# Performance work log

Measured on AMD Instinct MI355X. Metric: run time of the kernel, lower is better.

## Reference

```python
import jax, jax.numpy as jnp
import numpy as np
import math

C_CURV = 1.0          # manifold curvature c
KH = KW = 3
STRIDE = (1, 1)
PADDING = (1, 1)
DILATION = (1, 1)
IN_CH = 64            # includes time channel
OUT_CH = 64           # excludes time channel


def setup_inputs() -> dict:
    key = jax.random.key(0)
    k1, k2, k3 = jax.random.split(key, 3)
    B, H, W = 32, 64, 64
    x = jax.random.normal(k1, (B, H, W, IN_CH), dtype=jnp.float32)
    kk = KH * KW
    lin_in = (IN_CH - 1) * kk + 1  # 568
    stdv = math.sqrt(2.0 / ((IN_CH - 1) * kk))
    weight = jax.random.uniform(k2, (OUT_CH, lin_in), minval=-stdv, maxval=stdv, dtype=jnp.float32)
    bias = jax.random.uniform(k3, (OUT_CH,), minval=-stdv, maxval=stdv, dtype=jnp.float32)
    return {"x": x, "weight": weight, "bias": bias}


def _im2col(x):
    """x: [B,H,W,C] -> gathered patches [B,h_out,w_out,KH,KW,C] (torch Unfold semantics)."""
    B, H, W, C = x.shape
    xp = jnp.pad(x, ((0, 0), (PADDING[0], PADDING[0]), (PADDING[1], PADDING[1]), (0, 0)))
    h_out = (H + 2 * PADDING[0] - DILATION[0] * (KH - 1) - 1) // STRIDE[0] + 1
    w_out = (W + 2 * PADDING[1] - DILATION[1] * (KW - 1) - 1) // STRIDE[1] + 1
    rows = STRIDE[0] * jnp.arange(h_out)[:, None] + DILATION[0] * jnp.arange(KH)[None, :]  # [h_out,KH]
    cols = STRIDE[1] * jnp.arange(w_out)[:, None] + DILATION[1] * jnp.arange(KW)[None, :]  # [w_out,KW]
    g = xp[:, rows[:, None, :, None], cols[None, :, None, :], :]  # [B,h_out,w_out,KH,KW,C]
    return g, h_out, w_out


def reference(x, weight, bias):
    B = x.shape[0]
    kk = KH * KW
    g, h_out, w_out = _im2col(x)
    L = h_out * w_out
    # Time channel (channel 0) over kernel positions, clamped to sqrt(c)
    t = jnp.maximum(g[..., 0].reshape(B, L, kk), jnp.sqrt(jnp.float32(C_CURV)))
    t_rescaled = jnp.sqrt(jnp.sum(t * t, axis=-1, keepdims=True) - (kk - 1) * C_CURV)
    # Space channels in kernel-major, channel-minor order (matches torch reshape/transpose)
    s = g[..., 1:].reshape(B, L, kk * (IN_CH - 1))
    feat = jnp.concatenate([t_rescaled, s], axis=-1)  # [B, L, 568]
    # LorentzLinear: linear on features, recompute time from space norm
    y_space = jnp.einsum('blf,of->blo', feat, weight) + bias
    y_time = jnp.sqrt(jnp.sum(y_space * y_space, axis=-1, keepdims=True) + C_CURV)
    out = jnp.concatenate([y_time, y_space], axis=-1)
    return out.reshape(B, h_out, w_out, OUT_CH + 1)
```

## Files before the change

kernel.cpp:

```cpp
#include <hip/hip_runtime.h>
#include <cstdint>
#include <cstddef>

typedef __attribute__((ext_vector_type(4))) short short4v;
typedef __attribute__((ext_vector_type(8))) short short8v;
typedef __attribute__((ext_vector_type(4))) float floatx4;

#define LIN 568
#define KP  576

__device__ __forceinline__ short f32_to_bf16(float f) {
  unsigned u = __builtin_bit_cast(unsigned, f);
  u += 0x7fffu + ((u >> 16) & 1u);
  return (short)(u >> 16);
}
__device__ __forceinline__ float bf16_to_f32(short s) {
  unsigned u = ((unsigned)(unsigned short)s) << 16;
  return __builtin_bit_cast(float, u);
}

__global__ void prep_weight(const float* __restrict__ w, short* __restrict__ wbt) {
  int i = blockIdx.x * 256 + threadIdx.x;
  if (i >= 64 * KP) return;
  int n = i / KP;
  int k = i - n * KP;
  int tap = k >> 6;
  int c = k & 63;
  float v = (c == 0) ? 0.0f : w[n * LIN + 1 + tap * 63 + (c - 1)];
  wbt[i] = f32_to_bf16(v);
}

__launch_bounds__(512, 6)
__global__ void lconv_main(const float* __restrict__ x, const float* __restrict__ w,
                           const float* __restrict__ bias, const short* __restrict__ wbt,
                           float* __restrict__ out) {
  __shared__ short xt[4 * 66 * 72];
  __shared__ short wslab[64 * 72];
  __shared__ float tres[128];

  const int tid = threadIdx.x;
  const int bb = blockIdx.x >> 5;
  const int h0 = (blockIdx.x & 31) << 1;

  const float* xb = x + (size_t)bb * (64 * 64 * 64);

#pragma unroll
  for (int i = 0; i < 8; ++i) {
    int idx = i * 512 + tid;
    int row = idx >> 10;
    int rem = idx & 1023;
    int col = rem >> 4;
    int ch4 = (rem & 15) << 2;
    int h = h0 - 1 + row;
    float4 v = make_float4(0.f, 0.f, 0.f, 0.f);
    if ((unsigned)h < 64u) v = *(const float4*)(xb + (((h * 64 + col) * 64) + ch4));
    short4v o;
    o.x = f32_to_bf16(v.x); o.y = f32_to_bf16(v.y);
    o.z = f32_to_bf16(v.z); o.w = f32_to_bf16(v.w);
    *(short4v*)&xt[(row * 66 + col + 1) * 72 + ch4] = o;
  }
  if (tid < 128) {
    int r = tid >> 5;
    int cc = (tid >> 4) & 1;
    int ch4 = (tid & 15) << 2;
    short4v z = {0, 0, 0, 0};
    *(short4v*)&xt[(r * 66 + cc * 65) * 72 + ch4] = z;
  }
  __syncthreads();

  if (tid < 128) {
    int pr = tid >> 6, pc = tid & 63;
    float ss = 0.f;
#pragma unroll
    for (int dh = 0; dh < 3; ++dh)
#pragma unroll
      for (int dw = 0; dw < 3; ++dw) {
        float tv = bf16_to_f32(xt[((pr + dh) * 66 + pc + dw) * 72]);
        tv = fmaxf(tv, 1.0f);
        ss += tv * tv;
      }
    tres[tid] = sqrtf(ss - 8.0f);
  }

  const int lane = tid & 63;
  const int l15 = lane & 15;
  const int q = lane >> 4;
  const int wv = tid >> 6;
  const int pA = wv * 16 + l15;
  const int prA = pA >> 6;
  const int pcA = pA & 63;

  floatx4 acc0 = {0.f, 0.f, 0.f, 0.f};
  floatx4 acc1 = acc0, acc2 = acc0, acc3 = acc0;

  const int wn = tid >> 3;
  const int wpart = (tid & 7) << 3;

#pragma unroll
  for (int s = 0; s < 9; ++s) {
    short8v wv8 = *(const short8v*)(wbt + wn * KP + s * 64 + wpart);
    *(short8v*)&wslab[wn * 72 + wpart] = wv8;
    __syncthreads();

    const int kh = s / 3, kw = s % 3;
    const short* abase = &xt[((prA + kh) * 66 + (pcA + kw)) * 72];
#pragma unroll
    for (int half = 0; half < 2; ++half) {
      short8v af = *(const short8v*)(abase + half * 32 + q * 8);
      const short* bbase = &wslab[l15 * 72 + half * 32 + q * 8];
      short8v b0 = *(const short8v*)(bbase + 0 * 16 * 72);
      short8v b1 = *(const short8v*)(bbase + 1 * 16 * 72);
      short8v b2 = *(const short8v*)(bbase + 2 * 16 * 72);
      short8v b3 = *(const short8v*)(bbase + 3 * 16 * 72);
      acc0 = __builtin_amdgcn_mfma_f32_16x16x32_bf16(af, b0, acc0, 0, 0, 0);
      acc1 = __builtin_amdgcn_mfma_f32_16x16x32_bf16(af, b1, acc1, 0, 0, 0);
      acc2 = __builtin_amdgcn_mfma_f32_16x16x32_bf16(af, b2, acc2, 0, 0, 0);
      acc3 = __builtin_amdgcn_mfma_f32_16x16x32_bf16(af, b3, acc3, 0, 0, 0);
    }
    __syncthreads();
  }

  float bj[4], w0j[4];
#pragma unroll
  for (int j = 0; j < 4; ++j) {
    int n = j * 16 + l15;
    bj[j] = bias[n];
    w0j[j] = w[n * LIN];
  }
#pragma unroll
  for (int r = 0; r < 4; ++r) {
    int p = wv * 16 + q * 4 + r;
    float tr = tres[p];
    float v0 = acc0[r] + bj[0] + tr * w0j[0];
    float v1 = acc1[r] + bj[1] + tr * w0j[1];
    float v2 = acc2[r] + bj[2] + tr * w0j[2];
    float v3 = acc3[r] + bj[3] + tr * w0j[3];
    float ss = v0 * v0 + v1 * v1 + v2 * v2 + v3 * v3;
    ss += __shfl_xor(ss, 1);
    ss += __shfl_xor(ss, 2);
    ss += __shfl_xor(ss, 4);
    ss += __shfl_xor(ss, 8);
    int h = h0 + (p >> 6);
    int wc = p & 63;
    float* ob = out + (size_t)((bb * 64 + h) * 64 + wc) * 65;
    if (l15 == 0) ob[0] = sqrtf(ss + 1.0f);
    ob[1 + l15]  = v0;
    ob[17 + l15] = v1;
    ob[33 + l15] = v2;
    ob[49 + l15] = v3;
  }
}

extern "C" void kernel_launch(void* const* d_in, const int* in_sizes, int n_in,
                              void* d_out, int out_size, void* d_ws, size_t ws_size,
                              hipStream_t stream) {
  const float* x = (const float*)d_in[0];
  const float* w = (const float*)d_in[1];
  const float* b = (const float*)d_in[2];
  float* out = (float*)d_out;
  short* wbt = (short*)d_ws;

  prep_weight<<<(64 * KP + 255) / 256, 256, 0, stream>>>(w, wbt);
  lconv_main<<<32 * 32, 512, 0, stream>>>(x, w, b, wbt, out);
}
```

Measured before the change: 108.2 us.

## Pre-swizzle weights into MFMA fragments and enlarge per-wave output tile

The weight prep kernel now writes bf16 weights in MFMA B-fragment order, so each lane loads its fragments straight from global memory into registers. This removes the per-tap LDS weight slab and its two barriers per step. Each block now covers 4 output rows with 256 threads, and each wave computes a full 64-pixel row against all 64 outputs using a 4x4 accumulator tile, so every A and B fragment is reused four times. B fragments are prefetched two steps ahead; the cost is more accumulator registers, lower occupancy, and a larger LDS halo.

```diff
diff --git a/kernel.cpp b/kernel.cpp
--- a/kernel.cpp
+++ b/kernel.cpp
@@ -7,7 +7,6 @@
 typedef __attribute__((ext_vector_type(4))) float floatx4;
 
 #define LIN 568
-#define KP  576
 
 __device__ __forceinline__ short f32_to_bf16(float f) {
   unsigned u = __builtin_bit_cast(unsigned, f);
@@ -15,60 +14,66 @@
   return (short)(u >> 16);
 }
 __device__ __forceinline__ float bf16_to_f32(short s) {
-  unsigned u = ((unsigned)(unsigned short)s) << 16;
-  return __builtin_bit_cast(float, u);
+  return __builtin_bit_cast(float, ((unsigned)(unsigned short)s) << 16);
 }
 
-__global__ void prep_weight(const float* __restrict__ w, short* __restrict__ wbt) {
+__global__ void prep_weight(const float* __restrict__ w, short* __restrict__ wfragg) {
   int i = blockIdx.x * 256 + threadIdx.x;
-  if (i >= 64 * KP) return;
-  int n = i / KP;
-  int k = i - n * KP;
-  int tap = k >> 6;
-  int c = k & 63;
+  if (i >= 9 * 2 * 4 * 64 * 8) return;
+  int j    = i & 7;
+  int lane = (i >> 3) & 63;
+  int nb   = (i >> 9) & 3;
+  int half = (i >> 11) & 1;
+  int tap  = i >> 12;
+  int n = nb * 16 + (lane & 15);
+  int c = half * 32 + ((lane >> 4) << 3) + j;
   float v = (c == 0) ? 0.0f : w[n * LIN + 1 + tap * 63 + (c - 1)];
-  wbt[i] = f32_to_bf16(v);
+  wfragg[i] = f32_to_bf16(v);
 }
 
-__launch_bounds__(512, 6)
+__launch_bounds__(256, 2)
 __global__ void lconv_main(const float* __restrict__ x, const float* __restrict__ w,
-                           const float* __restrict__ bias, const short* __restrict__ wbt,
+                           const float* __restrict__ bias, const short* __restrict__ wfragg,
                            float* __restrict__ out) {
-  __shared__ short xt[4 * 66 * 72];
-  __shared__ short wslab[64 * 72];
-  __shared__ float tres[128];
+  __shared__ short xt[6 * 66 * 72];
+  __shared__ float tres[256];
 
   const int tid = threadIdx.x;
-  const int bb = blockIdx.x >> 5;
-  const int h0 = (blockIdx.x & 31) << 1;
-
+  const int bb = blockIdx.x >> 4;
+  const int h0 = (blockIdx.x & 15) << 2;
   const float* xb = x + (size_t)bb * (64 * 64 * 64);
 
 #pragma unroll
-  for (int i = 0; i < 8; ++i) {
-    int idx = i * 512 + tid;
-    int row = idx >> 10;
-    int rem = idx & 1023;
-    int col = rem >> 4;
-    int ch4 = (rem & 15) << 2;
+  for (int i = 0; i < 12; ++i) {
+    int idx = i * 256 + tid;
+    int row = idx >> 9;
+    int rem = idx & 511;
+    int col = rem >> 3;
+    int ch8 = (rem & 7) << 3;
     int h = h0 - 1 + row;
-    float4 v = make_float4(0.f, 0.f, 0.f, 0.f);
-    if ((unsigned)h < 64u) v = *(const float4*)(xb + (((h * 64 + col) * 64) + ch4));
-    short4v o;
-    o.x = f32_to_bf16(v.x); o.y = f32_to_bf16(v.y);
-    o.z = f32_to_bf16(v.z); o.w = f32_to_bf16(v.w);
-    *(short4v*)&xt[(row * 66 + col + 1) * 72 + ch4] = o;
+    float4 v0 = {0.f, 0.f, 0.f, 0.f}, v1 = {0.f, 0.f, 0.f, 0.f};
+    if ((unsigned)h < 64u) {
+      const float* p = xb + ((h * 64 + col) * 64 + ch8);
+      v0 = *(const float4*)p;
+      v1 = *(const float4*)(p + 4);
+    }
+    short8v o;
+    o[0] = f32_to_bf16(v0.x); o[1] = f32_to_bf16(v0.y);
+    o[2] = f32_to_bf16(v0.z); o[3] = f32_to_bf16(v0.w);
+    o[4] = f32_to_bf16(v1.x); o[5] = f32_to_bf16(v1.y);
+    o[6] = f32_to_bf16(v1.z); o[7] = f32_to_bf16(v1.w);
+    *(short8v*)&xt[(row * 66 + col + 1) * 72 + ch8] = o;
   }
-  if (tid < 128) {
-    int r = tid >> 5;
-    int cc = (tid >> 4) & 1;
-    int ch4 = (tid & 15) << 2;
-    short4v z = {0, 0, 0, 0};
-    *(short4v*)&xt[(r * 66 + cc * 65) * 72 + ch4] = z;
+  if (tid < 96) {
+    int r = tid >> 4;
+    int cc = (tid >> 3) & 1;
+    int ch8 = (tid & 7) << 3;
+    short8v z = {0, 0, 0, 0, 0, 0, 0, 0};
+    *(short8v*)&xt[(r * 66 + cc * 65) * 72 + ch8] = z;
   }
   __syncthreads();
 
-  if (tid < 128) {
+  {
     int pr = tid >> 6, pc = tid & 63;
     float ss = 0.f;
 #pragma unroll
@@ -86,68 +91,79 @@
   const int l15 = lane & 15;
   const int q = lane >> 4;
   const int wv = tid >> 6;
-  const int pA = wv * 16 + l15;
-  const int prA = pA >> 6;
-  const int pcA = pA & 63;
 
-  floatx4 acc0 = {0.f, 0.f, 0.f, 0.f};
-  floatx4 acc1 = acc0, acc2 = acc0, acc3 = acc0;
+  floatx4 acc[4][4];
+#pragma unroll
+  for (int mb = 0; mb < 4; ++mb)
+#pragma unroll
+    for (int nb = 0; nb < 4; ++nb) acc[mb][nb] = floatx4{0.f, 0.f, 0.f, 0.f};
 
-  const int wn = tid >> 3;
-  const int wpart = (tid & 7) << 3;
+  const short* wfl = wfragg + lane * 8;
+
+  short8v b0[4], b1[4];
+#pragma unroll
+  for (int nb = 0; nb < 4; ++nb) {
+    b0[nb] = *(const short8v*)(wfl + 0 * 2048 + nb * 512);
+    b1[nb] = *(const short8v*)(wfl + 1 * 2048 + nb * 512);
+  }
 
 #pragma unroll
-  for (int s = 0; s < 9; ++s) {
-    short8v wv8 = *(const short8v*)(wbt + wn * KP + s * 64 + wpart);
-    *(short8v*)&wslab[wn * 72 + wpart] = wv8;
-    __syncthreads();
+  for (int step = 0; step < 18; ++step) {
+    const int tap = step >> 1, half = step & 1;
+    const int kh = tap / 3, kw = tap % 3;
 
-    const int kh = s / 3, kw = s % 3;
-    const short* abase = &xt[((prA + kh) * 66 + (pcA + kw)) * 72];
+    short8v bn[4];
+    if (step + 2 < 18) {
 #pragma unroll
-    for (int half = 0; half < 2; ++half) {
-      short8v af = *(const short8v*)(abase + half * 32 + q * 8);
-      const short* bbase = &wslab[l15 * 72 + half * 32 + q * 8];
-      short8v b0 = *(const short8v*)(bbase + 0 * 16 * 72);
-      short8v b1 = *(const short8v*)(bbase + 1 * 16 * 72);
-      short8v b2 = *(const short8v*)(bbase + 2 * 16 * 72);
-      short8v b3 = *(const short8v*)(bbase + 3 * 16 * 72);
-      acc0 = __builtin_amdgcn_mfma_f32_16x16x32_bf16(af, b0, acc0, 0, 0, 0);
-      acc1 = __builtin_amdgcn_mfma_f32_16x16x32_bf16(af, b1, acc1, 0, 0, 0);
-      acc2 = __builtin_amdgcn_mfma_f32_16x16x32_bf16(af, b2, acc2, 0, 0, 0);
-      acc3 = __builtin_amdgcn_mfma_f32_16x16x32_bf16(af, b3, acc3, 0, 0, 0);
+      for (int nb = 0; nb < 4; ++nb)
+        bn[nb] = *(const short8v*)(wfl + (step + 2) * 2048 + nb * 512);
     }
-    __syncthreads();
+
+    const short* ab = &xt[((wv + kh) * 66 + kw + l15) * 72 + half * 32 + q * 8];
+    short8v a[4];
+#pragma unroll
+    for (int mb = 0; mb < 4; ++mb)
+      a[mb] = *(const short8v*)(ab + mb * 16 * 72);
+
+#pragma unroll
+    for (int mb = 0; mb < 4; ++mb) {
+#pragma unroll
+      for (int nb = 0; nb < 4; ++nb)
+        acc[mb][nb] = __builtin_amdgcn_mfma_f32_16x16x32_bf16(a[mb], b0[nb], acc[mb][nb], 0, 0, 0);
+    }
+#pragma unroll
+    for (int nb = 0; nb < 4; ++nb) { b0[nb] = b1[nb]; b1[nb] = bn[nb]; }
   }
 
   float bj[4], w0j[4];
 #pragma unroll
-  for (int j = 0; j < 4; ++j) {
-    int n = j * 16 + l15;
-    bj[j] = bias[n];
-    w0j[j] = w[n * LIN];
+  for (int nb = 0; nb < 4; ++nb) {
+    int n = nb * 16 + l15;
+    bj[nb] = bias[n];
+    w0j[nb] = w[n * LIN];
   }
 #pragma unroll
-  for (int r = 0; r < 4; ++r) {
-    int p = wv * 16 + q * 4 + r;
-    float tr = tres[p];
-    float v0 = acc0[r] + bj[0] + tr * w0j[0];
-    float v1 = acc1[r] + bj[1] + tr * w0j[1];
-    float v2 = acc2[r] + bj[2] + tr * w0j[2];
-    float v3 = acc3[r] + bj[3] + tr * w0j[3];
-    float ss = v0 * v0 + v1 * v1 + v2 * v2 + v3 * v3;
-    ss += __shfl_xor(ss, 1);
-    ss += __shfl_xor(ss, 2);
-    ss += __shfl_xor(ss, 4);
-    ss += __shfl_xor(ss, 8);
-    int h = h0 + (p >> 6);
-    int wc = p & 63;
-    float* ob = out + (size_t)((bb * 64 + h) * 64 + wc) * 65;
-    if (l15 == 0) ob[0] = sqrtf(ss + 1.0f);
-    ob[1 + l15]  = v0;
-    ob[17 + l15] = v1;
-    ob[33 + l15] = v2;
-    ob[49 + l15] = v3;
+  for (int mb = 0; mb < 4; ++mb) {
+#pragma unroll
+    for (int r = 0; r < 4; ++r) {
+      int pcol = mb * 16 + q * 4 + r;
+      float tr = tres[wv * 64 + pcol];
+      float v0 = acc[mb][0][r] + bj[0] + tr * w0j[0];
+      float v1 = acc[mb][1][r] + bj[1] + tr * w0j[1];
+      float v2 = acc[mb][2][r] + bj[2] + tr * w0j[2];
+      float v3 = acc[mb][3][r] + bj[3] + tr * w0j[3];
+      float ss = v0 * v0 + v1 * v1 + v2 * v2 + v3 * v3;
+      ss += __shfl_xor(ss, 1);
+      ss += __shfl_xor(ss, 2);
+      ss += __shfl_xor(ss, 4);
+      ss += __shfl_xor(ss, 8);
+      float* ob = out + (size_t)((bb * 64 + h0 + wv) * 64 + pcol) * 65;
+      if (l15 == 0) ob[0] = sqrtf(ss + 1.0f);
+      ob[1 + l15]  = v0;
+      ob[17 + l15] = v1;
+      ob[33 + l15] = v2;
+      ob[49 + l15] = v3;
+    }
   }
 }
 
@@ -158,8 +174,8 @@
   const float* w = (const float*)d_in[1];
   const float* b = (const float*)d_in[2];
   float* out = (float*)d_out;
-  short* wbt = (short*)d_ws;
+  short* wfragg = (short*)d_ws;
 
-  prep_weight<<<(64 * KP + 255) / 256, 256, 0, stream>>>(w, wbt);
-  lconv_main<<<32 * 32, 512, 0, stream>>>(x, w, b, wbt, out);
+  prep_weight<<<144, 256, 0, stream>>>(w, wfragg);
+  lconv_main<<<32 * 16, 256, 0, stream>>>(x, w, b, wfragg, out);
 }
```

Result: faster. 98.88 us (-8.6%).
